# Kernel tuning notes

Hardware: AMD Instinct MI355X
Metric: run time of the kernel (lower is better)

## Reference

```python
import jax, jax.numpy as jnp
import numpy as np

N_HEAD = 16
D_MODEL = 1024


def setup_inputs() -> dict:
    key = jax.random.key(0)
    ks = jax.random.split(key, 7)
    s = 1.0 / np.sqrt(D_MODEL)
    x = jax.random.normal(ks[0], (4, 2048, D_MODEL), dtype=jnp.float32)
    Wq = jax.random.uniform(ks[1], (D_MODEL, D_MODEL), jnp.float32, -s, s)
    Wk = jax.random.uniform(ks[2], (D_MODEL, D_MODEL), jnp.float32, -s, s)
    Wv = jax.random.uniform(ks[3], (D_MODEL, D_MODEL), jnp.float32, -s, s)
    bq = jax.random.uniform(ks[4], (D_MODEL,), jnp.float32, -s, s)
    bk = jax.random.uniform(ks[5], (D_MODEL,), jnp.float32, -s, s)
    bv = jax.random.uniform(ks[6], (D_MODEL,), jnp.float32, -s, s)
    gamma = jnp.ones((D_MODEL,), jnp.float32)
    beta = jnp.zeros((D_MODEL,), jnp.float32)
    return {"x": x, "Wq": Wq, "bq": bq, "Wk": Wk, "bk": bk, "Wv": Wv, "bv": bv,
            "gamma": gamma, "beta": beta}


def _layernorm(y, gamma, beta, eps=1e-5):
    mu = jnp.mean(y, axis=-1, keepdims=True)
    var = jnp.var(y, axis=-1, keepdims=True)
    return (y - mu) * jax.lax.rsqrt(var + eps) * gamma + beta


def reference(x, Wq, bq, Wk, bk, Wv, bv, gamma, beta):
    b, s, d = x.shape
    h = N_HEAD
    hd = d // h
    # projections -> [b, h, s, hd]
    def proj(W, bias):
        return (x @ W.T + bias).reshape(b, s, h, hd).transpose(0, 2, 1, 3)
    Q = proj(Wq, bq)
    K = proj(Wk, bk)
    V = proj(Wv, bv)
    scale = 1.0 / np.sqrt(hd)
    attn = jnp.einsum('bhqd,bhkd->bhqk', Q, K) * scale  # [b,h,s,s]
    attn = jax.nn.softmax(attn, axis=-1)
    ctx = jnp.einsum('bhqk,bhkd->bhqd', attn, V)
    ctx = ctx.transpose(0, 2, 1, 3).reshape(b, s, d)
    return _layernorm(ctx + x, gamma, beta)
```

## Files before the change

### kernel.cpp

```cpp
#include <hip/hip_runtime.h>
#include <stdint.h>

#define SEQ 2048
#define DM  1024
#define NH  16
#define HDIM 64

typedef __bf16 bf16x8 __attribute__((ext_vector_type(8)));
typedef __bf16 bf16x4 __attribute__((ext_vector_type(4)));
typedef float  f32x4  __attribute__((ext_vector_type(4)));
typedef unsigned int u32x2 __attribute__((ext_vector_type(2)));
typedef unsigned int u32x4 __attribute__((ext_vector_type(4)));

#define MFMA16(a,b,c) __builtin_amdgcn_mfma_f32_16x16x32_bf16((a),(b),(c),0,0,0)

#define QSCALE 0.18033688011112042f

__device__ __forceinline__ unsigned short f2bf(float f) {
  unsigned int u = __float_as_uint(f);
  u += 0x7fffu + ((u >> 16) & 1u);
  return (unsigned short)(u >> 16);
}

__device__ __forceinline__ void plane32(unsigned int& a, unsigned int& b) {
  asm("v_permlane32_swap_b32 %0, %1" : "+v"(a), "+v"(b));
}
__device__ __forceinline__ void plane16(unsigned int& a, unsigned int& b) {
  asm("v_permlane16_swap_b32 %0, %1" : "+v"(a), "+v"(b));
}

__device__ __forceinline__ void g2l16(const unsigned short* g, unsigned short* l) {
  __builtin_amdgcn_global_load_lds(
      (const __attribute__((address_space(1))) unsigned int*)g,
      (__attribute__((address_space(3))) unsigned int*)l, 16, 0, 0);
}

__global__ __launch_bounds__(256) void cast_all(
    const float* __restrict__ x, const float* __restrict__ wq,
    const float* __restrict__ wk, const float* __restrict__ wv,
    unsigned short* __restrict__ out) {
  const int nX = 4 * SEQ * DM, nW = DM * DM;
  int i = (blockIdx.x * 256 + threadIdx.x) * 4;
  const float* src;
  int off;
  if (i < nX)                { src = x;  off = i; }
  else if (i < nX + nW)      { src = wq; off = i - nX; }
  else if (i < nX + 2 * nW)  { src = wk; off = i - nX - nW; }
  else                       { src = wv; off = i - nX - 2 * nW; }
  float4 v = *(const float4*)(src + off);
  ushort4 o;
  o.x = f2bf(v.x); o.y = f2bf(v.y); o.z = f2bf(v.z); o.w = f2bf(v.w);
  *(ushort4*)(out + i) = o;
}

__global__ __launch_bounds__(256) void qkv_gemm(
    const unsigned short* __restrict__ X,
    const unsigned short* __restrict__ W0, const unsigned short* __restrict__ W1,
    const unsigned short* __restrict__ W2,
    const float* __restrict__ b0, const float* __restrict__ b1, const float* __restrict__ b2,
    unsigned short* __restrict__ O0, unsigned short* __restrict__ O1,
    unsigned short* __restrict__ O2)
{
  const int z = blockIdx.y >> 3;
  const unsigned short* W = (z == 0) ? W0 : (z == 1) ? W1 : W2;
  const float* bias = (z == 0) ? b0 : (z == 1) ? b1 : b2;
  unsigned short* Out = (z == 0) ? O0 : (z == 1) ? O1 : O2;
  const float scale = (z == 0) ? QSCALE : 1.0f;
  const bool vtrans = (z == 2);

  __shared__ unsigned short As[2][128 * 32];
  __shared__ unsigned short Bs[2][128 * 32];

  const int t = threadIdx.x;
  const int lane = t & 63;
  const int l15 = lane & 15, l4 = lane >> 4;
  const int w = t >> 6;
  const int wm = (w >> 1) * 64;
  const int wn = (w & 1) * 64;
  const int bm = blockIdx.x * 128;
  const int bn = (blockIdx.y & 7) * 128;

  const int cg = ((t & 3) ^ ((t >> 3) & 3)) * 8;
  const unsigned short* Ag = X + (size_t)(bm + (t >> 2)) * DM + cg;
  const unsigned short* Bg = W + (size_t)(bn + (t >> 2)) * DM + cg;

  f32x4 acc[4][4];
  #pragma unroll
  for (int mi = 0; mi < 4; mi++)
    #pragma unroll
    for (int ni = 0; ni < 4; ni++) acc[mi][ni] = (f32x4){0.f, 0.f, 0.f, 0.f};

  g2l16(Ag, &As[0][t * 8]);
  g2l16(Ag + 64 * DM, &As[0][2048 + t * 8]);
  g2l16(Bg, &Bs[0][t * 8]);
  g2l16(Bg + 64 * DM, &Bs[0][2048 + t * 8]);
  __syncthreads();

  const int fco = (l4 ^ ((l15 >> 1) & 3)) << 3;

  int cur = 0;
  for (int kt = 0; kt < DM; kt += 32) {
    if (kt + 32 < DM) {
      g2l16(Ag + kt + 32, &As[cur ^ 1][t * 8]);
      g2l16(Ag + kt + 32 + 64 * DM, &As[cur ^ 1][2048 + t * 8]);
      g2l16(Bg + kt + 32, &Bs[cur ^ 1][t * 8]);
      g2l16(Bg + kt + 32 + 64 * DM, &Bs[cur ^ 1][2048 + t * 8]);
    }

    bf16x8 af[4], bfr[4];
    #pragma unroll
    for (int mi = 0; mi < 4; mi++)
      af[mi] = *(const bf16x8*)&As[cur][(wm + mi * 16 + l15) * 32 + fco];
    #pragma unroll
    for (int ni = 0; ni < 4; ni++)
      bfr[ni] = *(const bf16x8*)&Bs[cur][(wn + ni * 16 + l15) * 32 + fco];
    if (!vtrans) {
      #pragma unroll
      for (int mi = 0; mi < 4; mi++)
        #pragma unroll
        for (int ni = 0; ni < 4; ni++)
          acc[mi][ni] = MFMA16(af[mi], bfr[ni], acc[mi][ni]);
    } else {
      #pragma unroll
      for (int mi = 0; mi < 4; mi++)
        #pragma unroll
        for (int ni = 0; ni < 4; ni++)
          acc[mi][ni] = MFMA16(bfr[ni], af[mi], acc[mi][ni]);
    }

    __syncthreads();
    cur ^= 1;
  }

  if (!vtrans) {
    #pragma unroll
    for (int ni = 0; ni < 4; ni++) {
      int n = bn + wn + ni * 16 + l15;
      float bv = bias[n];
      int h = n >> 6, hd = n & 63;
      #pragma unroll
      for (int mi = 0; mi < 4; mi++) {
        #pragma unroll
        for (int r = 0; r < 4; r++) {
          int m = bm + wm + mi * 16 + l4 * 4 + r;
          float v = (acc[mi][ni][r] + bv) * scale;
          int b = m >> 11, s = m & 2047;
          Out[(size_t)(b * NH + h) * (SEQ * HDIM) + (size_t)s * HDIM + hd] = f2bf(v);
        }
      }
    }
  } else {
    #pragma unroll
    for (int ni = 0; ni < 4; ni++) {
      #pragma unroll
      for (int r = 0; r < 4; r++) {
        int n = bn + wn + ni * 16 + l4 * 4 + r;
        float bv = bias[n];
        int h = n >> 6, hd = n & 63;
        #pragma unroll
        for (int mi = 0; mi < 4; mi++) {
          int m = bm + wm + mi * 16 + l15;
          float v = acc[mi][ni][r] + bv;
          int b = m >> 11, s = m & 2047;
          Out[(size_t)(b * NH + h) * (SEQ * HDIM) + (size_t)hd * SEQ + s] = f2bf(v);
        }
      }
    }
  }
}

__global__ __launch_bounds__(256) void attn_kernel(
    const unsigned short* __restrict__ Qg,
    const unsigned short* __restrict__ Kg,
    const unsigned short* __restrict__ Vg,
    unsigned short* __restrict__ ctxb)
{
  __shared__ unsigned short Klds[2][64 * 64];
  __shared__ unsigned short Vlds[2][64 * 64];

  const f32x4 ZERO4 = {0.f, 0.f, 0.f, 0.f};

  const int t = threadIdx.x;
  const int lane = t & 63;
  const int w = t >> 6;
  const int l15 = lane & 15, l4 = lane >> 4;
  const int bh = blockIdx.x;
  const int qt = blockIdx.y;

  const unsigned short* Q = Qg + (size_t)bh * SEQ * HDIM;
  const unsigned short* K = Kg + (size_t)bh * SEQ * HDIM;
  const unsigned short* V = Vg + (size_t)bh * HDIM * SEQ;

  const int q0 = qt * 128 + w * 32;

  bf16x8 qf[2][2];
  #pragma unroll
  for (int qi = 0; qi < 2; qi++)
    #pragma unroll
    for (int ks = 0; ks < 2; ks++)
      qf[qi][ks] = *(const bf16x8*)&Q[(size_t)(q0 + qi * 16 + l15) * HDIM + ks * 32 + l4 * 8];

  const __bf16 ob = (l15 == 0) ? (__bf16)1.0f : (__bf16)0.0f;
  const bf16x8 onesf = {ob, ob, ob, ob, ob, ob, ob, ob};

  f32x4 o[4][2];
  f32x4 psum[2];
  #pragma unroll
  for (int hdi = 0; hdi < 4; hdi++)
    #pragma unroll
    for (int qi = 0; qi < 2; qi++) o[hdi][qi] = ZERO4;
  #pragma unroll
  for (int qi = 0; qi < 2; qi++) psum[qi] = ZERO4;

  const int r0 = t >> 3, c0 = t & 7;
  const int scw = (c0 ^ (r0 & 7)) * 8;
  const unsigned short* KgS = K + (size_t)r0 * HDIM + scw;
  const unsigned short* VgS = V + (size_t)r0 * SEQ + scw;

  const int sw = l15 & 7;
  int fboff[2];
  #pragma unroll
  for (int ks = 0; ks < 2; ks++)
    fboff[ks] = l15 * 64 + (((ks * 4 + l4) ^ sw) << 3);

  g2l16(KgS, &Klds[0][t * 8]);
  g2l16(KgS + 32 * HDIM, &Klds[0][2048 + t * 8]);
  g2l16(VgS, &Vlds[0][t * 8]);
  g2l16(VgS + 32 * SEQ, &Vlds[0][2048 + t * 8]);
  __syncthreads();

  int cur = 0;
  for (int kt = 0; kt < SEQ; kt += 64) {
    if (kt + 64 < SEQ) {
      const unsigned short* kn = KgS + (size_t)(kt + 64) * HDIM;
      const unsigned short* vn = VgS + (kt + 64);
      g2l16(kn, &Klds[cur ^ 1][t * 8]);
      g2l16(kn + 32 * HDIM, &Klds[cur ^ 1][2048 + t * 8]);
      g2l16(vn, &Vlds[cur ^ 1][t * 8]);
      g2l16(vn + 32 * SEQ, &Vlds[cur ^ 1][2048 + t * 8]);
    }

    const unsigned short* Kc = Klds[cur];
    const unsigned short* Vc = Vlds[cur];

    #pragma unroll
    for (int u = 0; u < 2; u++) {
      unsigned int pw[2][4];
      #pragma unroll
      for (int half = 0; half < 2; half++) {
        const int slab = u * 2 + half;
        bf16x8 kf0 = *(const bf16x8*)(Kc + fboff[0] + slab * 1024);
        bf16x8 kf1 = *(const bf16x8*)(Kc + fboff[1] + slab * 1024);
        f32x4 sacc[2];
        __builtin_amdgcn_s_setprio(1);
        #pragma unroll
        for (int qi = 0; qi < 2; qi++) {
          sacc[qi] = MFMA16(kf0, qf[qi][0], ZERO4);
          sacc[qi] = MFMA16(kf1, qf[qi][1], sacc[qi]);
        }
        __builtin_amdgcn_s_setprio(0);
        #pragma unroll
        for (int qi = 0; qi < 2; qi++) {
          float p0 = __builtin_amdgcn_exp2f(sacc[qi][0]);
          float p1 = __builtin_amdgcn_exp2f(sacc[qi][1]);
          float p2 = __builtin_amdgcn_exp2f(sacc[qi][2]);
          float p3 = __builtin_amdgcn_exp2f(sacc[qi][3]);
          bf16x4 pb = {(__bf16)p0, (__bf16)p1, (__bf16)p2, (__bf16)p3};
          u32x2 pu = __builtin_bit_cast(u32x2, pb);
          pw[qi][half * 2 + 0] = pu.x;
          pw[qi][half * 2 + 1] = pu.y;
        }
      }

      bf16x8 pfrag[2];
      #pragma unroll
      for (int qi = 0; qi < 2; qi++) {
        unsigned int a0 = pw[qi][0], b0 = pw[qi][1];
        unsigned int a1 = pw[qi][2], b1 = pw[qi][3];
        plane32(a0, a1);
        plane32(b0, b1);
        plane16(a0, a1);
        plane16(b0, b1);
        u32x4 uw = {a0, b0, a1, b1};
        pfrag[qi] = __builtin_bit_cast(bf16x8, uw);
      }

      bf16x8 vf[4];
      #pragma unroll
      for (int hdi = 0; hdi < 4; hdi++)
        vf[hdi] = *(const bf16x8*)(Vc + fboff[u] + hdi * 1024);

      __builtin_amdgcn_s_setprio(1);
      #pragma unroll
      for (int qi = 0; qi < 2; qi++)
        psum[qi] = MFMA16(onesf, pfrag[qi], psum[qi]);
      #pragma unroll
      for (int hdi = 0; hdi < 4; hdi++)
        #pragma unroll
        for (int qi = 0; qi < 2; qi++)
          o[hdi][qi] = MFMA16(vf[hdi], pfrag[qi], o[hdi][qi]);
      __builtin_amdgcn_s_setprio(0);
    }

    __syncthreads();
    cur ^= 1;
  }

  float inv[2];
  #pragma unroll
  for (int qi = 0; qi < 2; qi++) inv[qi] = 1.0f / __shfl(psum[qi][0], l15);

  const int b = bh >> 4, h = bh & 15;
  #pragma unroll
  for (int hdi = 0; hdi < 4; hdi++)
    #pragma unroll
    for (int qi = 0; qi < 2; qi++) {
      int srow = q0 + qi * 16 + l15;
      f32x4 val = o[hdi][qi] * inv[qi];
      bf16x4 vk = {(__bf16)val[0], (__bf16)val[1], (__bf16)val[2], (__bf16)val[3]};
      *(bf16x4*)&ctxb[(size_t)(b * SEQ + srow) * DM + h * HDIM + hdi * 16 + l4 * 4] = vk;
    }
}

__global__ __launch_bounds__(256) void ln_kernel(const unsigned short* __restrict__ ctxb,
                                                 const float* __restrict__ x,
                                                 const float* __restrict__ gamma,
                                                 const float* __restrict__ beta,
                                                 float* __restrict__ out)
{
  const int row = blockIdx.x;
  const int t = threadIdx.x;
  const float* xr = x + (size_t)row * DM;
  float* orow = out + (size_t)row * DM;

  ushort4 cu = *(const ushort4*)(ctxb + (size_t)row * DM + t * 4);
  float4 xv = *(const float4*)(xr + t * 4);
  float v[4];
  v[0] = __uint_as_float((unsigned)cu.x << 16) + xv.x;
  v[1] = __uint_as_float((unsigned)cu.y << 16) + xv.y;
  v[2] = __uint_as_float((unsigned)cu.z << 16) + xv.z;
  v[3] = __uint_as_float((unsigned)cu.w << 16) + xv.w;
  float s = v[0] + v[1] + v[2] + v[3];
  float q = v[0] * v[0] + v[1] * v[1] + v[2] * v[2] + v[3] * v[3];
  #pragma unroll
  for (int off = 1; off < 64; off <<= 1) {
    s += __shfl_xor(s, off);
    q += __shfl_xor(q, off);
  }
  __shared__ float sh[8];
  int w = t >> 6, lane = t & 63;
  if (lane == 0) { sh[w] = s; sh[4 + w] = q; }
  __syncthreads();
  s = sh[0] + sh[1] + sh[2] + sh[3];
  q = sh[4] + sh[5] + sh[6] + sh[7];
  float mu = s * (1.0f / DM);
  float var = q * (1.0f / DM) - mu * mu;
  float rstd = rsqrtf(var + 1e-5f);
  float4 g = *(const float4*)(gamma + t * 4);
  float4 bt = *(const float4*)(beta + t * 4);
  float4 ov;
  ov.x = (v[0] - mu) * rstd * g.x + bt.x;
  ov.y = (v[1] - mu) * rstd * g.y + bt.y;
  ov.z = (v[2] - mu) * rstd * g.z + bt.z;
  ov.w = (v[3] - mu) * rstd * g.w + bt.w;
  *(float4*)(orow + t * 4) = ov;
}

extern "C" void kernel_launch(void* const* d_in, const int* in_sizes, int n_in,
                              void* d_out, int out_size, void* d_ws, size_t ws_size,
                              hipStream_t stream) {
  const float* x     = (const float*)d_in[0];
  const float* Wq    = (const float*)d_in[1];
  const float* bq    = (const float*)d_in[2];
  const float* Wk    = (const float*)d_in[3];
  const float* bk    = (const float*)d_in[4];
  const float* Wv    = (const float*)d_in[5];
  const float* bv    = (const float*)d_in[6];
  const float* gamma = (const float*)d_in[7];
  const float* beta  = (const float*)d_in[8];
  float* out = (float*)d_out;

  const int nX = 4 * SEQ * DM;
  const int nW = DM * DM;

  unsigned short* ws  = (unsigned short*)d_ws;
  unsigned short* Xb  = ws;
  unsigned short* Wqb = Xb + nX;
  unsigned short* Wkb = Wqb + nW;
  unsigned short* Wvb = Wkb + nW;
  unsigned short* Qg  = Wvb + nW;
  unsigned short* Kg  = Qg + nX;
  unsigned short* Vg  = Kg + nX;

  cast_all<<<(nX + 3 * nW) / 1024, 256, 0, stream>>>(x, Wq, Wk, Wv, Xb);
  qkv_gemm<<<dim3(64, 24), 256, 0, stream>>>(
      Xb, Wqb, Wkb, Wvb, bq, bk, bv, Qg, Kg, Vg);
  attn_kernel<<<dim3(4 * NH, SEQ / 128), 256, 0, stream>>>(Qg, Kg, Vg, Xb);
  ln_kernel<<<4 * SEQ, 256, 0, stream>>>(Xb, x, gamma, beta, out);
}
```

Baseline: 277.1 us.

## Triple-buffer QKV GEMM LDS with explicit vmcnt waits and one barrier

```diff
diff --git a/kernel.cpp b/kernel.cpp
--- a/kernel.cpp
+++ b/kernel.cpp
@@ -68,8 +68,8 @@
   const float scale = (z == 0) ? QSCALE : 1.0f;
   const bool vtrans = (z == 2);
 
-  __shared__ unsigned short As[2][128 * 32];
-  __shared__ unsigned short Bs[2][128 * 32];
+  __shared__ unsigned short As[3][128 * 32];
+  __shared__ unsigned short Bs[3][128 * 32];
 
   const int t = threadIdx.x;
   const int lane = t & 63;
@@ -90,30 +90,39 @@
     #pragma unroll
     for (int ni = 0; ni < 4; ni++) acc[mi][ni] = (f32x4){0.f, 0.f, 0.f, 0.f};
 
-  g2l16(Ag, &As[0][t * 8]);
-  g2l16(Ag + 64 * DM, &As[0][2048 + t * 8]);
-  g2l16(Bg, &Bs[0][t * 8]);
-  g2l16(Bg + 64 * DM, &Bs[0][2048 + t * 8]);
-  __syncthreads();
-
   const int fco = (l4 ^ ((l15 >> 1) & 3)) << 3;
 
+  #define STAGE(tile, buf)                                            \
+    do {                                                              \
+      g2l16(Ag + (tile) * 32, &As[(buf)][t * 8]);                     \
+      g2l16(Ag + (tile) * 32 + 64 * DM, &As[(buf)][2048 + t * 8]);    \
+      g2l16(Bg + (tile) * 32, &Bs[(buf)][t * 8]);                     \
+      g2l16(Bg + (tile) * 32 + 64 * DM, &Bs[(buf)][2048 + t * 8]);    \
+    } while (0)
+
+  STAGE(0, 0);
+  STAGE(1, 1);
+
+  const int NSTEP = DM / 32;
   int cur = 0;
-  for (int kt = 0; kt < DM; kt += 32) {
-    if (kt + 32 < DM) {
-      g2l16(Ag + kt + 32, &As[cur ^ 1][t * 8]);
-      g2l16(Ag + kt + 32 + 64 * DM, &As[cur ^ 1][2048 + t * 8]);
-      g2l16(Bg + kt + 32, &Bs[cur ^ 1][t * 8]);
-      g2l16(Bg + kt + 32 + 64 * DM, &Bs[cur ^ 1][2048 + t * 8]);
-    }
-
+  int nb = 2;
+  for (int kt = 0; kt < NSTEP; kt++) {
+    if (kt == NSTEP - 1)
+      asm volatile("s_waitcnt vmcnt(0)" ::: "memory");
+    else
+      asm volatile("s_waitcnt vmcnt(4)" ::: "memory");
+    __builtin_amdgcn_s_barrier();
+    if (kt + 2 < NSTEP) STAGE(kt + 2, nb);
+
+    const unsigned short* Ac = As[cur];
+    const unsigned short* Bc = Bs[cur];
     bf16x8 af[4], bfr[4];
     #pragma unroll
     for (int mi = 0; mi < 4; mi++)
-      af[mi] = *(const bf16x8*)&As[cur][(wm + mi * 16 + l15) * 32 + fco];
+      af[mi] = *(const bf16x8*)&Ac[(wm + mi * 16 + l15) * 32 + fco];
     #pragma unroll
     for (int ni = 0; ni < 4; ni++)
-      bfr[ni] = *(const bf16x8*)&Bs[cur][(wn + ni * 16 + l15) * 32 + fco];
+      bfr[ni] = *(const bf16x8*)&Bc[(wn + ni * 16 + l15) * 32 + fco];
     if (!vtrans) {
       #pragma unroll
       for (int mi = 0; mi < 4; mi++)
@@ -128,9 +137,10 @@
           acc[mi][ni] = MFMA16(bfr[ni], af[mi], acc[mi][ni]);
     }
 
-    __syncthreads();
-    cur ^= 1;
+    cur = (cur == 2) ? 0 : cur + 1;
+    nb = (nb == 2) ? 0 : nb + 1;
   }
+  #undef STAGE
 
   if (!vtrans) {
     #pragma unroll
```

Result: faster. 270.7 us (-2.3%).
